# Kernel tuning notes

Hardware: AMD Instinct MI355X
Metric: run time of the kernel (lower is better)

The kernel has to match this reference:

```python
import jax, jax.numpy as jnp
import numpy as np
from jax import lax

B, N, F_IN, T = 4, 30000, 2, 12
HID, HORIZON, E = 32, 12, 240000


def setup_inputs() -> dict:
    key = jax.random.key(0)
    ks = jax.random.split(key, 20)

    def lin_init(k, fan_in, shape):
        b = 1.0 / np.sqrt(fan_in)
        return jax.random.uniform(k, shape, jnp.float32, -b, b)

    def glorot(k, shape):
        b = np.sqrt(6.0 / (shape[0] + shape[1]))
        return jax.random.uniform(k, shape, jnp.float32, -b, b)

    return {
        "x": jax.random.normal(ks[0], (B, N, F_IN, T), jnp.float32),
        "edge_index": jax.random.randint(ks[1], (2, E), 0, N, jnp.int32),
        # A3TGCN2 attention over periods (init: uniform[0,1))
        "attention": jax.random.uniform(ks[2], (T,), jnp.float32),
        # TGCN2 gates: GCNConv weight (F_IN,HID) + bias, Linear (2*HID,HID) + bias
        "conv_z_w": glorot(ks[3], (F_IN, HID)), "conv_z_b": jnp.zeros((HID,), jnp.float32),
        "lin_z_w": lin_init(ks[4], 2 * HID, (2 * HID, HID)), "lin_z_b": lin_init(ks[5], 2 * HID, (HID,)),
        "conv_r_w": glorot(ks[6], (F_IN, HID)), "conv_r_b": jnp.zeros((HID,), jnp.float32),
        "lin_r_w": lin_init(ks[7], 2 * HID, (2 * HID, HID)), "lin_r_b": lin_init(ks[8], 2 * HID, (HID,)),
        "conv_h_w": glorot(ks[9], (F_IN, HID)), "conv_h_b": jnp.zeros((HID,), jnp.float32),
        "lin_h_w": lin_init(ks[10], 2 * HID, (2 * HID, HID)), "lin_h_b": lin_init(ks[11], 2 * HID, (HID,)),
        # trailing head Linear(HID, HORIZON)
        "head_w": lin_init(ks[12], HID, (HID, HORIZON)), "head_b": lin_init(ks[13], HID, (HORIZON,)),
    }


def _forward(x, attention, conv_z_w, conv_z_b, lin_z_w, lin_z_b,
             conv_r_w, conv_r_b, lin_r_w, lin_r_b,
             conv_h_w, conv_h_b, lin_h_w, lin_h_b,
             head_w, head_b, edge_index):
    b, n = x.shape[0], x.shape[1]
    # GCN normalization with added self loops: D^-1/2 (A+I) D^-1/2
    loop = jnp.arange(n, dtype=edge_index.dtype)
    src = jnp.concatenate([edge_index[0], loop])  # (E+N,) message sources
    dst = jnp.concatenate([edge_index[1], loop])  # (E+N,) message targets
    deg = jnp.zeros((n,), x.dtype).at[dst].add(1.0)  # deg >= 1 due to self loops
    dinv = lax.rsqrt(deg)
    norm = dinv[src] * dinv[dst]  # (E+N,)

    def gcn(xt, W, bias):
        # xt: (B,N,F) -> (B,N,HID); gather from src, scatter-add to dst
        xw = jnp.einsum('bnf,fh->bnh', xt, W)
        msg = xw[:, src, :] * norm[None, :, None]  # (B,E+N,HID)
        agg = jnp.zeros((b, n, W.shape[1]), xt.dtype).at[:, dst, :].add(msg)
        return agg + bias

    probs = jax.nn.softmax(attention)  # (T,)
    H0 = jnp.zeros((b, n, HID), x.dtype)  # A3TGCN2 passes H=None every period

    def step(acc, inps):
        xt, p = inps  # xt: (B,N,F)
        Z = jax.nn.sigmoid(jnp.concatenate([gcn(xt, conv_z_w, conv_z_b), H0], -1) @ lin_z_w + lin_z_b)
        R = jax.nn.sigmoid(jnp.concatenate([gcn(xt, conv_r_w, conv_r_b), H0], -1) @ lin_r_w + lin_r_b)
        Ht = jnp.tanh(jnp.concatenate([gcn(xt, conv_h_w, conv_h_b), H0 * R], -1) @ lin_h_w + lin_h_b)
        Hn = Z * H0 + (1.0 - Z) * Ht
        return acc + p * Hn, None

    acc, _ = lax.scan(step, H0, (jnp.moveaxis(x, 3, 0), probs))
    return jax.nn.relu(acc) @ head_w + head_b  # (B,N,HORIZON)


def reference(x, edge_index, attention, conv_z_w, conv_z_b, lin_z_w, lin_z_b,
              conv_r_w, conv_r_b, lin_r_w, lin_r_b,
              conv_h_w, conv_h_b, lin_h_w, lin_h_b, head_w, head_b):
    return _forward(x, attention, conv_z_w, conv_z_b, lin_z_w, lin_z_b,
                    conv_r_w, conv_r_b, lin_r_w, lin_r_b,
                    conv_h_w, conv_h_b, lin_h_w, lin_h_b,
                    head_w, head_b, edge_index)
```

## Files before the change

kernel.cpp:

```cpp
#include <hip/hip_runtime.h>

#define BB   4
#define NN   30000
#define TT   12
#define EE   240000
#define FT   24
#define NM   96
#define CAP  32
#define OVCAP 2048
#define FB   ((EE + 1023) / 1024)
#define LOG2E 1.44269504088896340736f

#define WS_CNT 0
#define WS_OVC 30000
#define WS_EFF 30016
#define WS_OVF 30272
#define WS_BKT 34368

__device__ __forceinline__ float readlane_f(float v, int l) {
    return __int_as_float(__builtin_amdgcn_readlane(__float_as_int(v), l));
}

__global__ void __launch_bounds__(256)
k_pre(const int* __restrict__ src, const int* __restrict__ dst,
      const float* __restrict__ czw, const float* __restrict__ czb,
      const float* __restrict__ lzw, const float* __restrict__ lzb,
      const float* __restrict__ chw, const float* __restrict__ chb,
      const float* __restrict__ lhw, const float* __restrict__ lhb,
      const float* __restrict__ att,
      int* __restrict__ cnt, int* __restrict__ ovc,
      int* __restrict__ ovf, int* __restrict__ bucket, float* __restrict__ eff) {
    int bid = blockIdx.x, lt = threadIdx.x;
    if (bid < FB) {
        int e = bid * 1024 + lt * 4;
        if (e < EE) {
            int4 s4 = *(const int4*)(src + e);
            int4 d4 = *(const int4*)(dst + e);
            int sl0 = atomicAdd(&cnt[d4.x], 1);
            int sl1 = atomicAdd(&cnt[d4.y], 1);
            int sl2 = atomicAdd(&cnt[d4.z], 1);
            int sl3 = atomicAdd(&cnt[d4.w], 1);
            if (sl0 < CAP) bucket[d4.x * CAP + sl0] = s4.x;
            else { int o = atomicAdd(ovc, 1); if (o < OVCAP) { ovf[2*o] = d4.x; ovf[2*o+1] = s4.x; } }
            if (sl1 < CAP) bucket[d4.y * CAP + sl1] = s4.y;
            else { int o = atomicAdd(ovc, 1); if (o < OVCAP) { ovf[2*o] = d4.y; ovf[2*o+1] = s4.y; } }
            if (sl2 < CAP) bucket[d4.z * CAP + sl2] = s4.z;
            else { int o = atomicAdd(ovc, 1); if (o < OVCAP) { ovf[2*o] = d4.z; ovf[2*o+1] = s4.z; } }
            if (sl3 < CAP) bucket[d4.w * CAP + sl3] = s4.w;
            else { int o = atomicAdd(ovc, 1); if (o < OVCAP) { ovf[2*o] = d4.w; ovf[2*o+1] = s4.w; } }
        }
        return;
    }
    int j = lt;
    if (j < 32) {
        float wz0 = 0.f, wz1 = 0.f, bz = 0.f, wh0 = 0.f, wh1 = 0.f, bh = 0.f;
        for (int k = 0; k < 32; ++k) {
            float lz = lzw[k * 32 + j], lh = lhw[k * 32 + j];
            wz0 = fmaf(czw[k],      lz, wz0);
            wz1 = fmaf(czw[32 + k], lz, wz1);
            bz  = fmaf(czb[k],      lz, bz);
            wh0 = fmaf(chw[k],      lh, wh0);
            wh1 = fmaf(chw[32 + k], lh, wh1);
            bh  = fmaf(chb[k],      lh, bh);
        }
        eff[j]        = -LOG2E * wz0;
        eff[32 + j]   = -LOG2E * wz1;
        eff[64 + j]   = -LOG2E * (bz + lzb[j]);
        eff[96 + j]   = 2.0f * LOG2E * wh0;
        eff[128 + j]  = 2.0f * LOG2E * wh1;
        eff[160 + j]  = 2.0f * LOG2E * (bh + lhb[j]);
    } else if (j == 32) {
        float m = -1e30f;
        for (int t = 0; t < TT; ++t) m = fmaxf(m, att[t]);
        float p[TT], s = 0.f;
        for (int t = 0; t < TT; ++t) { p[t] = __expf(att[t] - m); s += p[t]; }
        float inv = 1.0f / s;
        for (int t = 0; t < TT; ++t) eff[192 + t] = p[t] * inv;
    }
}

__global__ void __launch_bounds__(256)
k_fused(const float* __restrict__ x, const int* __restrict__ cnt,
        const int* __restrict__ ovc, const int* __restrict__ ovf,
        const int* __restrict__ bucket, const float* __restrict__ eff,
        const float* __restrict__ hw, const float* __restrict__ hb,
        float* __restrict__ out) {
    __shared__ __align__(16) float shwT[12 * 36];
    __shared__ float shb[12];
    __shared__ __align__(16) float sx[4 * NM];
    __shared__ __align__(16) float lacc[4 * 144];
    const int lt = threadIdx.x, lane = lt & 63, w = lt >> 6;
    const int n = blockIdx.x * 4 + w;

    int bval = 0;
    if (lane < CAP) bval = bucket[n * CAP + lane];
    const int cn  = cnt[n];
    const int nov0 = *ovc;

    const int j = lane & 31;
    const float az0 = eff[j],      az1 = eff[32 + j],  ab = eff[64 + j];
    const float ch0 = eff[96 + j], ch1 = eff[128 + j], cb = eff[160 + j];
    float pt[TT];
#pragma unroll
    for (int t = 0; t < TT; ++t) pt[t] = eff[192 + t];

#pragma unroll
    for (int i = 0; i < 6; ++i) {
        int idx = lane + 64 * i;
        int jj = idx / 12, kk = idx - 12 * jj;
        shwT[kk * 36 + jj] = hw[idx];
    }
    if (lane < 12) shb[lane] = hb[lane];

    const bool act = (lane < 48);
    const int b = lane / 12, f2 = lane - 12 * b;
    const float2* xb = (const float2*)x;
    const int lane_off = b * (NN * 12) + f2;

    const int bv2 = ((unsigned)bval < (unsigned)NN) ? bval : n;
    int cv = 0;
    if (lane < CAP) cv = cnt[bv2];

    const int deg = __builtin_amdgcn_readfirstlane(cn);
    const int m = (deg < CAP) ? deg : CAP;
    const int mp1 = m + 1;
    const int sv = (lane < m) ? bv2 : n;
    const int cc = (lane < m) ? cv : deg;
    const float wv = (lane <= m) ? rsqrtf((float)(cc + 1)) : 0.f;

    float2 acc = {0.f, 0.f};
    {
        const float2* P[12];
#pragma unroll
        for (int i = 0; i < 12; ++i) {
            int si = __builtin_amdgcn_readlane(sv, i);
            P[i] = xb + (size_t)si * 12;
        }
        if (act) {
            float2 v0  = P[0][lane_off],  v1  = P[1][lane_off];
            float2 v2  = P[2][lane_off],  v3  = P[3][lane_off];
            float2 v4  = P[4][lane_off],  v5  = P[5][lane_off];
            float2 v6  = P[6][lane_off],  v7  = P[7][lane_off];
            float2 v8  = P[8][lane_off],  v9  = P[9][lane_off];
            float2 v10 = P[10][lane_off], v11 = P[11][lane_off];
            float w0 = readlane_f(wv, 0),  w1 = readlane_f(wv, 1);
            float w2 = readlane_f(wv, 2),  w3 = readlane_f(wv, 3);
            float w4 = readlane_f(wv, 4),  w5 = readlane_f(wv, 5);
            float w6 = readlane_f(wv, 6),  w7 = readlane_f(wv, 7);
            float w8 = readlane_f(wv, 8),  w9 = readlane_f(wv, 9);
            float w10 = readlane_f(wv, 10), w11 = readlane_f(wv, 11);
            acc.x = fmaf(w0, v0.x, acc.x);   acc.y = fmaf(w0, v0.y, acc.y);
            acc.x = fmaf(w1, v1.x, acc.x);   acc.y = fmaf(w1, v1.y, acc.y);
            acc.x = fmaf(w2, v2.x, acc.x);   acc.y = fmaf(w2, v2.y, acc.y);
            acc.x = fmaf(w3, v3.x, acc.x);   acc.y = fmaf(w3, v3.y, acc.y);
            acc.x = fmaf(w4, v4.x, acc.x);   acc.y = fmaf(w4, v4.y, acc.y);
            acc.x = fmaf(w5, v5.x, acc.x);   acc.y = fmaf(w5, v5.y, acc.y);
            acc.x = fmaf(w6, v6.x, acc.x);   acc.y = fmaf(w6, v6.y, acc.y);
            acc.x = fmaf(w7, v7.x, acc.x);   acc.y = fmaf(w7, v7.y, acc.y);
            acc.x = fmaf(w8, v8.x, acc.x);   acc.y = fmaf(w8, v8.y, acc.y);
            acc.x = fmaf(w9, v9.x, acc.x);   acc.y = fmaf(w9, v9.y, acc.y);
            acc.x = fmaf(w10, v10.x, acc.x); acc.y = fmaf(w10, v10.y, acc.y);
            acc.x = fmaf(w11, v11.x, acc.x); acc.y = fmaf(w11, v11.y, acc.y);
        }
    }
    for (int k = 12; k < mp1; k += 4) {
        int s0 = __builtin_amdgcn_readlane(sv, k);
        int s1 = __builtin_amdgcn_readlane(sv, k + 1);
        int s2 = __builtin_amdgcn_readlane(sv, k + 2);
        int s3 = __builtin_amdgcn_readlane(sv, k + 3);
        const float2* p0 = xb + (size_t)s0 * 12;
        const float2* p1 = xb + (size_t)s1 * 12;
        const float2* p2 = xb + (size_t)s2 * 12;
        const float2* p3 = xb + (size_t)s3 * 12;
        if (act) {
            float2 v0 = p0[lane_off], v1 = p1[lane_off];
            float2 v2 = p2[lane_off], v3 = p3[lane_off];
            float w0 = readlane_f(wv, k),     w1 = readlane_f(wv, k + 1);
            float w2 = readlane_f(wv, k + 2), w3 = readlane_f(wv, k + 3);
            acc.x = fmaf(w0, v0.x, acc.x); acc.y = fmaf(w0, v0.y, acc.y);
            acc.x = fmaf(w1, v1.x, acc.x); acc.y = fmaf(w1, v1.y, acc.y);
            acc.x = fmaf(w2, v2.x, acc.x); acc.y = fmaf(w2, v2.y, acc.y);
            acc.x = fmaf(w3, v3.x, acc.x); acc.y = fmaf(w3, v3.y, acc.y);
        }
    }

    int nov = __builtin_amdgcn_readfirstlane(nov0);
    if (nov > 0) {
        if (nov > OVCAP) nov = OVCAP;
        for (int i = 0; i < nov; ++i) {
            int d = ovf[2 * i];
            if (d == n) {
                int s = ovf[2 * i + 1];
                float ws_ = rsqrtf((float)(cnt[s] + 1));
                if (act) {
                    float2 v = xb[lane_off + s * 12];
                    acc.x = fmaf(ws_, v.x, acc.x);
                    acc.y = fmaf(ws_, v.y, acc.y);
                }
            }
        }
    }

    const float dn = readlane_f(wv, m);
    if (act) {
        float* sxw = sx + w * NM + b * FT;
        const int g = (f2 < 6) ? (4 * f2) : (4 * (f2 - 6) + 1);
        sxw[g]     = dn * acc.x;
        sxw[g + 2] = dn * acc.y;
    }

    asm volatile("s_waitcnt lgkmcnt(0)" ::: "memory");

    const int b0_ = lane >> 5;
#pragma unroll
    for (int bi = 0; bi < 2; ++bi) {
        const int bb = b0_ + 2 * bi;
        const float4* srow4 = (const float4*)(sx + w * NM + bb * FT);
        float a0 = 0.f, a1 = 0.f;
#pragma unroll
        for (int tp = 0; tp < 6; ++tp) {
            float4 s4 = srow4[tp];
            float aeX = fmaf(s4.y, az1, fmaf(s4.x, az0, ab));
            float aeY = fmaf(s4.w, az1, fmaf(s4.z, az0, ab));
            float ceX = fmaf(s4.y, ch1, fmaf(s4.x, ch0, cb));
            float ceY = fmaf(s4.w, ch1, fmaf(s4.z, ch0, cb));
            aeX = fminf(fmaxf(aeX, -60.f), 60.f);
            aeY = fminf(fmaxf(aeY, -60.f), 60.f);
            ceX = fminf(fmaxf(ceX, -60.f), 60.f);
            ceY = fminf(fmaxf(ceY, -60.f), 60.f);
            float uX  = __builtin_amdgcn_exp2f(aeX);
            float uY  = __builtin_amdgcn_exp2f(aeY);
            float eX  = __builtin_amdgcn_exp2f(ceX);
            float eY  = __builtin_amdgcn_exp2f(ceY);
            float t1X = 1.0f + uX,  t1Y = 1.0f + uY;
            float dX  = fmaf(eX, t1X, t1X), dY = fmaf(eY, t1Y, t1Y);
            float nX  = fmaf(uX, eX, -uX),  nY = fmaf(uY, eY, -uY);
            float rX  = __builtin_amdgcn_rcpf(dX);
            float rY  = __builtin_amdgcn_rcpf(dY);
            a0 = fmaf(pt[2 * tp] * nX, rX, a0);
            a1 = fmaf(pt[2 * tp + 1] * nY, rY, a1);
        }
        lacc[w * 144 + bb * 36 + j] = fmaxf(a0 + a1, 0.f);
    }
    asm volatile("s_waitcnt lgkmcnt(0)" ::: "memory");

    if (lane < 48) {
        int bb = lane / 12, kk = lane - 12 * bb;
        float r = shb[kk];
        const float4* la4 = (const float4*)(lacc + w * 144 + bb * 36);
        const float4* wt4 = (const float4*)(shwT + kk * 36);
#pragma unroll
        for (int q = 0; q < 8; ++q) {
            float4 A = la4[q], W = wt4[q];
            r = fmaf(A.x, W.x, r); r = fmaf(A.y, W.y, r);
            r = fmaf(A.z, W.z, r); r = fmaf(A.w, W.w, r);
        }
        out[((long long)bb * NN + n) * 12 + kk] = r;
    }
}

extern "C" void kernel_launch(void* const* d_in, const int* in_sizes, int n_in,
                              void* d_out, int out_size, void* d_ws, size_t ws_size,
                              hipStream_t stream) {
    const float* x   = (const float*)d_in[0];
    const int*   ei  = (const int*)d_in[1];
    const float* att = (const float*)d_in[2];
    const float* czw = (const float*)d_in[3];
    const float* czb = (const float*)d_in[4];
    const float* lzw = (const float*)d_in[5];
    const float* lzb = (const float*)d_in[6];
    const float* chw = (const float*)d_in[11];
    const float* chb = (const float*)d_in[12];
    const float* lhw = (const float*)d_in[13];
    const float* lhb = (const float*)d_in[14];
    const float* hw  = (const float*)d_in[15];
    const float* hb  = (const float*)d_in[16];
    float* out = (float*)d_out;

    float* ws = (float*)d_ws;
    int*   cnt = (int*)(ws + WS_CNT);
    int*   ovc = (int*)(ws + WS_OVC);
    float* eff = ws + WS_EFF;
    int*   ovf = (int*)(ws + WS_OVF);
    int*   bkt = (int*)(ws + WS_BKT);

    const int* src = ei;
    const int* dst = ei + EE;

    hipMemsetAsync(cnt, 0, WS_EFF * 4, stream);
    k_pre<<<FB + 1, 256, 0, stream>>>(src, dst, czw, czb, lzw, lzb,
                                      chw, chb, lhw, lhb, att,
                                      cnt, ovc, ovf, bkt, eff);
    k_fused<<<NN / 4, 256, 0, stream>>>(x, cnt, ovc, ovf, bkt, eff, hw, hb, out);
}
```

Before: 136.3 us.

## Process four nodes per wavefront with software-pipelined neighbor gathers

Each wavefront now handles four consecutive nodes instead of one. The bucket/count loads for the next node are prefetched, and the x-gather for node i+1 is issued before node i's gate math and head matmul. This hides gather latency and amortizes the per-block setup (weight transposes, eff loads) over more nodes. It also simplifies the exponent clamping to a one-sided min and scalarizes the attention probabilities with readfirstlane. The costs are higher register pressure and fewer blocks, which reduces occupancy.

After: 139.6 us. +2.4%, slower.

```diff
diff --git a/kernel.cpp b/kernel.cpp
--- a/kernel.cpp
+++ b/kernel.cpp
@@ -10,6 +10,7 @@
 #define OVCAP 2048
 #define FB   ((EE + 1023) / 1024)
 #define LOG2E 1.44269504088896340736f
+#define NPW  4
 
 #define WS_CNT 0
 #define WS_OVC 30000
@@ -19,6 +20,9 @@
 
 __device__ __forceinline__ float readlane_f(float v, int l) {
     return __int_as_float(__builtin_amdgcn_readlane(__float_as_int(v), l));
+}
+__device__ __forceinline__ float rfl_f(float v) {
+    return __int_as_float(__builtin_amdgcn_readfirstlane(__float_as_int(v)));
 }
 
 __global__ void __launch_bounds__(256)
@@ -90,11 +94,13 @@
     __shared__ __align__(16) float sx[4 * NM];
     __shared__ __align__(16) float lacc[4 * 144];
     const int lt = threadIdx.x, lane = lt & 63, w = lt >> 6;
-    const int n = blockIdx.x * 4 + w;
-
-    int bval = 0;
-    if (lane < CAP) bval = bucket[n * CAP + lane];
-    const int cn  = cnt[n];
+    const int nbase = (blockIdx.x * 4 + w) * NPW;
+
+    int bval[NPW + 2], cn_[NPW + 2];
+    bval[0] = 0; if (lane < CAP) bval[0] = bucket[(nbase + 0) * CAP + lane];
+    cn_[0] = cnt[nbase + 0];
+    bval[1] = 0; if (lane < CAP) bval[1] = bucket[(nbase + 1) * CAP + lane];
+    cn_[1] = cnt[nbase + 1];
     const int nov0 = *ovc;
 
     const int j = lane & 31;
@@ -102,7 +108,7 @@
     const float ch0 = eff[96 + j], ch1 = eff[128 + j], cb = eff[160 + j];
     float pt[TT];
 #pragma unroll
-    for (int t = 0; t < TT; ++t) pt[t] = eff[192 + t];
+    for (int t = 0; t < TT; ++t) pt[t] = rfl_f(eff[192 + t]);
 
 #pragma unroll
     for (int i = 0; i < 6; ++i) {
@@ -116,146 +122,154 @@
     const int b = lane / 12, f2 = lane - 12 * b;
     const float2* xb = (const float2*)x;
     const int lane_off = b * (NN * 12) + f2;
-
-    const int bv2 = ((unsigned)bval < (unsigned)NN) ? bval : n;
-    int cv = 0;
-    if (lane < CAP) cv = cnt[bv2];
-
-    const int deg = __builtin_amdgcn_readfirstlane(cn);
-    const int m = (deg < CAP) ? deg : CAP;
-    const int mp1 = m + 1;
-    const int sv = (lane < m) ? bv2 : n;
-    const int cc = (lane < m) ? cv : deg;
-    const float wv = (lane <= m) ? rsqrtf((float)(cc + 1)) : 0.f;
-
-    float2 acc = {0.f, 0.f};
+    float* const sxw = sx + w * NM + b * FT;
+    const int g = (f2 < 6) ? (4 * f2) : (4 * (f2 - 6) + 1);
+    const int b0_ = lane >> 5;
+
+    int bv2[NPW + 1], cv[NPW + 1], sv[NPW + 1], mm[NPW + 1];
+    float wvv[NPW + 1];
+    float2 xv[12];
+
+    bv2[0] = ((unsigned)bval[0] < (unsigned)NN) ? bval[0] : (nbase + 0);
+    cv[0] = 0; if (lane < CAP) cv[0] = cnt[bv2[0]];
     {
+        const int deg = __builtin_amdgcn_readfirstlane(cn_[0]);
+        mm[0] = (deg < CAP) ? deg : CAP;
+        sv[0] = (lane < mm[0]) ? bv2[0] : (nbase + 0);
+        const int cc = (lane < mm[0]) ? cv[0] : deg;
+        wvv[0] = (lane <= mm[0]) ? rsqrtf((float)(cc + 1)) : 0.f;
         const float2* P[12];
 #pragma unroll
-        for (int i = 0; i < 12; ++i) {
-            int si = __builtin_amdgcn_readlane(sv, i);
-            P[i] = xb + (size_t)si * 12;
-        }
+        for (int q = 0; q < 12; ++q)
+            P[q] = xb + (size_t)__builtin_amdgcn_readlane(sv[0], q) * 12;
         if (act) {
-            float2 v0  = P[0][lane_off],  v1  = P[1][lane_off];
-            float2 v2  = P[2][lane_off],  v3  = P[3][lane_off];
-            float2 v4  = P[4][lane_off],  v5  = P[5][lane_off];
-            float2 v6  = P[6][lane_off],  v7  = P[7][lane_off];
-            float2 v8  = P[8][lane_off],  v9  = P[9][lane_off];
-            float2 v10 = P[10][lane_off], v11 = P[11][lane_off];
-            float w0 = readlane_f(wv, 0),  w1 = readlane_f(wv, 1);
-            float w2 = readlane_f(wv, 2),  w3 = readlane_f(wv, 3);
-            float w4 = readlane_f(wv, 4),  w5 = readlane_f(wv, 5);
-            float w6 = readlane_f(wv, 6),  w7 = readlane_f(wv, 7);
-            float w8 = readlane_f(wv, 8),  w9 = readlane_f(wv, 9);
-            float w10 = readlane_f(wv, 10), w11 = readlane_f(wv, 11);
-            acc.x = fmaf(w0, v0.x, acc.x);   acc.y = fmaf(w0, v0.y, acc.y);
-            acc.x = fmaf(w1, v1.x, acc.x);   acc.y = fmaf(w1, v1.y, acc.y);
-            acc.x = fmaf(w2, v2.x, acc.x);   acc.y = fmaf(w2, v2.y, acc.y);
-            acc.x = fmaf(w3, v3.x, acc.x);   acc.y = fmaf(w3, v3.y, acc.y);
-            acc.x = fmaf(w4, v4.x, acc.x);   acc.y = fmaf(w4, v4.y, acc.y);
-            acc.x = fmaf(w5, v5.x, acc.x);   acc.y = fmaf(w5, v5.y, acc.y);
-            acc.x = fmaf(w6, v6.x, acc.x);   acc.y = fmaf(w6, v6.y, acc.y);
-            acc.x = fmaf(w7, v7.x, acc.x);   acc.y = fmaf(w7, v7.y, acc.y);
-            acc.x = fmaf(w8, v8.x, acc.x);   acc.y = fmaf(w8, v8.y, acc.y);
-            acc.x = fmaf(w9, v9.x, acc.x);   acc.y = fmaf(w9, v9.y, acc.y);
-            acc.x = fmaf(w10, v10.x, acc.x); acc.y = fmaf(w10, v10.y, acc.y);
-            acc.x = fmaf(w11, v11.x, acc.x); acc.y = fmaf(w11, v11.y, acc.y);
-        }
-    }
-    for (int k = 12; k < mp1; k += 4) {
-        int s0 = __builtin_amdgcn_readlane(sv, k);
-        int s1 = __builtin_amdgcn_readlane(sv, k + 1);
-        int s2 = __builtin_amdgcn_readlane(sv, k + 2);
-        int s3 = __builtin_amdgcn_readlane(sv, k + 3);
-        const float2* p0 = xb + (size_t)s0 * 12;
-        const float2* p1 = xb + (size_t)s1 * 12;
-        const float2* p2 = xb + (size_t)s2 * 12;
-        const float2* p3 = xb + (size_t)s3 * 12;
+#pragma unroll
+            for (int q = 0; q < 12; ++q) xv[q] = P[q][lane_off];
+        }
+    }
+
+#pragma unroll
+    for (int i = 0; i < NPW; ++i) {
+        const int n = nbase + i;
+        if (i + 1 < NPW) {
+            bv2[i+1] = ((unsigned)bval[i+1] < (unsigned)NN) ? bval[i+1] : (n + 1);
+            cv[i+1] = 0; if (lane < CAP) cv[i+1] = cnt[bv2[i+1]];
+        }
+        if (i + 2 < NPW) {
+            bval[i+2] = 0; if (lane < CAP) bval[i+2] = bucket[(nbase + i + 2) * CAP + lane];
+            cn_[i+2] = cnt[nbase + i + 2];
+        }
+        float2 acc = {0.f, 0.f};
         if (act) {
-            float2 v0 = p0[lane_off], v1 = p1[lane_off];
-            float2 v2 = p2[lane_off], v3 = p3[lane_off];
-            float w0 = readlane_f(wv, k),     w1 = readlane_f(wv, k + 1);
-            float w2 = readlane_f(wv, k + 2), w3 = readlane_f(wv, k + 3);
-            acc.x = fmaf(w0, v0.x, acc.x); acc.y = fmaf(w0, v0.y, acc.y);
-            acc.x = fmaf(w1, v1.x, acc.x); acc.y = fmaf(w1, v1.y, acc.y);
-            acc.x = fmaf(w2, v2.x, acc.x); acc.y = fmaf(w2, v2.y, acc.y);
-            acc.x = fmaf(w3, v3.x, acc.x); acc.y = fmaf(w3, v3.y, acc.y);
-        }
-    }
-
-    int nov = __builtin_amdgcn_readfirstlane(nov0);
-    if (nov > 0) {
-        if (nov > OVCAP) nov = OVCAP;
-        for (int i = 0; i < nov; ++i) {
-            int d = ovf[2 * i];
-            if (d == n) {
-                int s = ovf[2 * i + 1];
-                float ws_ = rsqrtf((float)(cnt[s] + 1));
-                if (act) {
-                    float2 v = xb[lane_off + s * 12];
-                    acc.x = fmaf(ws_, v.x, acc.x);
-                    acc.y = fmaf(ws_, v.y, acc.y);
+#pragma unroll
+            for (int q = 0; q < 12; ++q) {
+                float wq = readlane_f(wvv[i], q);
+                acc.x = fmaf(wq, xv[q].x, acc.x);
+                acc.y = fmaf(wq, xv[q].y, acc.y);
+            }
+        }
+        const int mp1 = mm[i] + 1;
+        for (int k = 12; k < mp1; k += 4) {
+            int s0 = __builtin_amdgcn_readlane(sv[i], k);
+            int s1 = __builtin_amdgcn_readlane(sv[i], k + 1);
+            int s2 = __builtin_amdgcn_readlane(sv[i], k + 2);
+            int s3 = __builtin_amdgcn_readlane(sv[i], k + 3);
+            const float2* p0 = xb + (size_t)s0 * 12;
+            const float2* p1 = xb + (size_t)s1 * 12;
+            const float2* p2 = xb + (size_t)s2 * 12;
+            const float2* p3 = xb + (size_t)s3 * 12;
+            if (act) {
+                float2 v0 = p0[lane_off], v1 = p1[lane_off];
+                float2 v2 = p2[lane_off], v3 = p3[lane_off];
+                float w0 = readlane_f(wvv[i], k),     w1 = readlane_f(wvv[i], k + 1);
+                float w2 = readlane_f(wvv[i], k + 2), w3 = readlane_f(wvv[i], k + 3);
+                acc.x = fmaf(w0, v0.x, acc.x); acc.y = fmaf(w0, v0.y, acc.y);
+                acc.x = fmaf(w1, v1.x, acc.x); acc.y = fmaf(w1, v1.y, acc.y);
+                acc.x = fmaf(w2, v2.x, acc.x); acc.y = fmaf(w2, v2.y, acc.y);
+                acc.x = fmaf(w3, v3.x, acc.x); acc.y = fmaf(w3, v3.y, acc.y);
+            }
+        }
+        int nov = __builtin_amdgcn_readfirstlane(nov0);
+        if (nov > 0) {
+            if (nov > OVCAP) nov = OVCAP;
+            for (int o = 0; o < nov; ++o) {
+                int d = ovf[2 * o];
+                if (d == n) {
+                    int s = ovf[2 * o + 1];
+                    float ws_ = rsqrtf((float)(cnt[s] + 1));
+                    if (act) {
+                        float2 v = xb[lane_off + s * 12];
+                        acc.x = fmaf(ws_, v.x, acc.x);
+                        acc.y = fmaf(ws_, v.y, acc.y);
+                    }
                 }
             }
         }
-    }
-
-    const float dn = readlane_f(wv, m);
-    if (act) {
-        float* sxw = sx + w * NM + b * FT;
-        const int g = (f2 < 6) ? (4 * f2) : (4 * (f2 - 6) + 1);
-        sxw[g]     = dn * acc.x;
-        sxw[g + 2] = dn * acc.y;
-    }
-
-    asm volatile("s_waitcnt lgkmcnt(0)" ::: "memory");
-
-    const int b0_ = lane >> 5;
-#pragma unroll
-    for (int bi = 0; bi < 2; ++bi) {
-        const int bb = b0_ + 2 * bi;
-        const float4* srow4 = (const float4*)(sx + w * NM + bb * FT);
-        float a0 = 0.f, a1 = 0.f;
-#pragma unroll
-        for (int tp = 0; tp < 6; ++tp) {
-            float4 s4 = srow4[tp];
-            float aeX = fmaf(s4.y, az1, fmaf(s4.x, az0, ab));
-            float aeY = fmaf(s4.w, az1, fmaf(s4.z, az0, ab));
-            float ceX = fmaf(s4.y, ch1, fmaf(s4.x, ch0, cb));
-            float ceY = fmaf(s4.w, ch1, fmaf(s4.z, ch0, cb));
-            aeX = fminf(fmaxf(aeX, -60.f), 60.f);
-            aeY = fminf(fmaxf(aeY, -60.f), 60.f);
-            ceX = fminf(fmaxf(ceX, -60.f), 60.f);
-            ceY = fminf(fmaxf(ceY, -60.f), 60.f);
-            float uX  = __builtin_amdgcn_exp2f(aeX);
-            float uY  = __builtin_amdgcn_exp2f(aeY);
-            float eX  = __builtin_amdgcn_exp2f(ceX);
-            float eY  = __builtin_amdgcn_exp2f(ceY);
-            float t1X = 1.0f + uX,  t1Y = 1.0f + uY;
-            float dX  = fmaf(eX, t1X, t1X), dY = fmaf(eY, t1Y, t1Y);
-            float nX  = fmaf(uX, eX, -uX),  nY = fmaf(uY, eY, -uY);
-            float rX  = __builtin_amdgcn_rcpf(dX);
-            float rY  = __builtin_amdgcn_rcpf(dY);
-            a0 = fmaf(pt[2 * tp] * nX, rX, a0);
-            a1 = fmaf(pt[2 * tp + 1] * nY, rY, a1);
-        }
-        lacc[w * 144 + bb * 36 + j] = fmaxf(a0 + a1, 0.f);
-    }
-    asm volatile("s_waitcnt lgkmcnt(0)" ::: "memory");
-
-    if (lane < 48) {
-        int bb = lane / 12, kk = lane - 12 * bb;
-        float r = shb[kk];
-        const float4* la4 = (const float4*)(lacc + w * 144 + bb * 36);
-        const float4* wt4 = (const float4*)(shwT + kk * 36);
-#pragma unroll
-        for (int q = 0; q < 8; ++q) {
-            float4 A = la4[q], W = wt4[q];
-            r = fmaf(A.x, W.x, r); r = fmaf(A.y, W.y, r);
-            r = fmaf(A.z, W.z, r); r = fmaf(A.w, W.w, r);
-        }
-        out[((long long)bb * NN + n) * 12 + kk] = r;
+        const float dn = readlane_f(wvv[i], mm[i]);
+        if (act) {
+            sxw[g]     = dn * acc.x;
+            sxw[g + 2] = dn * acc.y;
+        }
+        if (i + 1 < NPW) {
+            const int deg = __builtin_amdgcn_readfirstlane(cn_[i+1]);
+            mm[i+1] = (deg < CAP) ? deg : CAP;
+            sv[i+1] = (lane < mm[i+1]) ? bv2[i+1] : (n + 1);
+            const int cc = (lane < mm[i+1]) ? cv[i+1] : deg;
+            wvv[i+1] = (lane <= mm[i+1]) ? rsqrtf((float)(cc + 1)) : 0.f;
+            const float2* P[12];
+#pragma unroll
+            for (int q = 0; q < 12; ++q)
+                P[q] = xb + (size_t)__builtin_amdgcn_readlane(sv[i+1], q) * 12;
+            if (act) {
+#pragma unroll
+                for (int q = 0; q < 12; ++q) xv[q] = P[q][lane_off];
+            }
+        }
+        asm volatile("s_waitcnt lgkmcnt(0)" ::: "memory");
+
+#pragma unroll
+        for (int bi = 0; bi < 2; ++bi) {
+            const int bb = b0_ + 2 * bi;
+            const float4* srow4 = (const float4*)(sx + w * NM + bb * FT);
+            float a0 = 0.f, a1 = 0.f;
+#pragma unroll
+            for (int tp = 0; tp < 6; ++tp) {
+                float4 s4 = srow4[tp];
+                float aeX = fmaf(s4.y, az1, fmaf(s4.x, az0, ab));
+                float aeY = fmaf(s4.w, az1, fmaf(s4.z, az0, ab));
+                float ceX = fmaf(s4.y, ch1, fmaf(s4.x, ch0, cb));
+                float ceY = fmaf(s4.w, ch1, fmaf(s4.z, ch0, cb));
+                aeX = fminf(aeX, 24.f); aeY = fminf(aeY, 24.f);
+                ceX = fminf(ceX, 24.f); ceY = fminf(ceY, 24.f);
+                float uX  = __builtin_amdgcn_exp2f(aeX);
+                float uY  = __builtin_amdgcn_exp2f(aeY);
+                float eX  = __builtin_amdgcn_exp2f(ceX);
+                float eY  = __builtin_amdgcn_exp2f(ceY);
+                float t1X = 1.0f + uX,  t1Y = 1.0f + uY;
+                float dX  = fmaf(eX, t1X, t1X), dY = fmaf(eY, t1Y, t1Y);
+                float nX  = fmaf(uX, eX, -uX),  nY = fmaf(uY, eY, -uY);
+                float rX  = __builtin_amdgcn_rcpf(dX);
+                float rY  = __builtin_amdgcn_rcpf(dY);
+                a0 = fmaf(pt[2 * tp] * nX, rX, a0);
+                a1 = fmaf(pt[2 * tp + 1] * nY, rY, a1);
+            }
+            lacc[w * 144 + bb * 36 + j] = fmaxf(a0 + a1, 0.f);
+        }
+        asm volatile("s_waitcnt lgkmcnt(0)" ::: "memory");
+
+        if (lane < 48) {
+            int bb = lane / 12, kk = lane - 12 * bb;
+            float r = shb[kk];
+            const float4* la4 = (const float4*)(lacc + w * 144 + bb * 36);
+            const float4* wt4 = (const float4*)(shwT + kk * 36);
+#pragma unroll
+            for (int q = 0; q < 8; ++q) {
+                float4 A = la4[q], W = wt4[q];
+                r = fmaf(A.x, W.x, r); r = fmaf(A.y, W.y, r);
+                r = fmaf(A.z, W.z, r); r = fmaf(A.w, W.w, r);
+            }
+            out[((long long)bb * NN + n) * 12 + kk] = r;
+        }
     }
 }
 
@@ -291,5 +305,5 @@
     k_pre<<<FB + 1, 256, 0, stream>>>(src, dst, czw, czb, lzw, lzb,
                                       chw, chb, lhw, lhb, att,
                                       cnt, ovc, ovf, bkt, eff);
-    k_fused<<<NN / 4, 256, 0, stream>>>(x, cnt, ovc, ovf, bkt, eff, hw, hb, out);
-}
+    k_fused<<<NN / (4 * NPW), 256, 0, stream>>>(x, cnt, ovc, ovf, bkt, eff, hw, hb, out);
+}
```
